# Performance work log

Measured on AMD Instinct MI355X. Metric: run time of the kernel, lower is better.

The kernel has to match this reference:

```python
import jax, jax.numpy as jnp
import numpy as np

NBINS = 100  # hard-coded in torch.histogram(first, 100)


def setup_inputs() -> dict:
    key = jax.random.key(0)
    k1, k2 = jax.random.split(key)
    z = jax.random.normal(k1, (100000, 16), dtype=jnp.float32)
    cluster_layer = jax.random.normal(k2, (16, 16), dtype=jnp.float32)
    return {"z": z, "cluster_layer": cluster_layer}


def _per_feature_hist(combined):
    """Equal-width per-feature histogram (torch.histogram(x, 100) semantics).
    combined: [N+C, F] -> edges [F, NBINS+1], counts [F, NBINS] (float)."""
    lo = combined.min(axis=0)          # [F]
    hi = combined.max(axis=0)          # [F]
    t = jnp.linspace(0.0, 1.0, NBINS + 1, dtype=combined.dtype)  # [NBINS+1]
    edges = lo[:, None] + (hi - lo)[:, None] * t[None, :]        # [F, NBINS+1]
    # bin assignment: left-closed bins, last bin right-closed (np/torch histogram)
    idx = jax.vmap(lambda e, v: jnp.searchsorted(e, v, side="right"),
                   in_axes=(0, 1))(edges, combined) - 1          # [F, N+C]
    idx = jnp.clip(idx, 0, NBINS - 1)
    counts = jax.vmap(lambda i: jnp.zeros((NBINS,), combined.dtype).at[i].add(1.0))(idx)
    return edges, counts


def _mass_dissimilarity(z, cluster_layer):
    N, F = z.shape
    C = cluster_layer.shape[0]
    combined = jax.lax.stop_gradient(jnp.concatenate([z, cluster_layer], axis=0))  # detach()
    edges, counts = _per_feature_hist(combined)          # [F,101], [F,100]

    # searchsorted(bins, .) - 1, per feature (side='left' like torch default)
    sample_bins = jax.vmap(lambda e, v: jnp.searchsorted(e, v, side="left"),
                           in_axes=(0, 1))(edges, z).T - 1              # [N, F]
    cluster_bins = jax.vmap(lambda e, v: jnp.searchsorted(e, v, side="left"),
                            in_axes=(0, 1))(edges, cluster_layer).T - 1  # [C, F]

    mx = jnp.maximum(sample_bins[:, None, :], cluster_bins[None, :, :])  # [N, C, F]
    mn = jnp.minimum(sample_bins[:, None, :], cluster_bins[None, :, :])  # [N, C, F]

    cum = jnp.cumsum(counts, axis=1)                     # [F, NBINS]
    f_idx = jnp.arange(F)                                # broadcasts over [N, C, F]
    is_zero = mn <= 0
    lo_idx = jnp.where(is_zero, 0, mn - 1)
    lo_sum = cum[f_idx, lo_idx]                          # [N, C, F]
    hi_sum = cum[f_idx, jnp.clip(mx, 0, NBINS - 1)]      # [N, C, F]
    sum_counts = jnp.where(is_zero, hi_sum, hi_sum - lo_sum)

    divisor = jnp.asarray(N + C, z.dtype)
    # len(counts)==1 in the original after reshape(1,1,F,NBINS), so no extra divide
    mass = jnp.sqrt(jnp.sum((sum_counts / divisor) ** 2, axis=2))  # [N, C]
    return mass


def reference(z, cluster_layer):
    # get_Q(z, 'mass'): q = 1/(1+mass), row-normalized
    q = 1.0 / (1.0 + _mass_dissimilarity(z, cluster_layer))
    q = q / jnp.sum(q, axis=1, keepdims=True)
    return q
```

## Files before the change

### kernel.cpp

```cpp
#include <hip/hip_runtime.h>
#include <stdint.h>

#define NBINS 100
#define FF 16
#define CC 16
#define MM_BLOCKS 256
#define HIST_BLOCKS 256


__device__ __forceinline__ unsigned enc_f(float v) {
    unsigned u = __float_as_uint(v);
    return (u & 0x80000000u) ? ~u : (u | 0x80000000u);
}
__device__ __forceinline__ float dec_f(unsigned e) {
    unsigned u = (e & 0x80000000u) ? (e ^ 0x80000000u) : ~e;
    return __uint_as_float(u);
}
__device__ __forceinline__ unsigned shfl_xor_u(unsigned x, int m) {
    return (unsigned)__shfl_xor((int)x, m, 64);
}
__device__ __forceinline__ float edgeval(float lo, float d, int k) {
    float tt = (k == NBINS) ? 1.0f : __fmul_rn((float)k, 0.01f);
    return __fadd_rn(lo, __fmul_rn(d, tt));
}

__global__ __launch_bounds__(256) void k_minmax(const float4* __restrict__ z4,
                                                const float4* __restrict__ cl4,
                                                int zn4, int total4,
                                                unsigned* __restrict__ partials,
                                                unsigned* __restrict__ counts) {
    int gtid = blockIdx.x * 256 + threadIdx.x;
    if (gtid < FF * NBINS) counts[gtid] = 0u;

    unsigned mn[4] = {~0u, ~0u, ~0u, ~0u}, mx[4] = {0u, 0u, 0u, 0u};
    int stride = MM_BLOCKS * 256;
    for (int i = gtid; i < total4; i += stride) {
        float4 v = (i < zn4) ? z4[i] : cl4[i - zn4];
        unsigned e;
        e = enc_f(v.x); mn[0] = min(mn[0], e); mx[0] = max(mx[0], e);
        e = enc_f(v.y); mn[1] = min(mn[1], e); mx[1] = max(mx[1], e);
        e = enc_f(v.z); mn[2] = min(mn[2], e); mx[2] = max(mx[2], e);
        e = enc_f(v.w); mn[3] = min(mn[3], e); mx[3] = max(mx[3], e);
    }
#pragma unroll
    for (int off = 4; off < 64; off <<= 1) {
#pragma unroll
        for (int c = 0; c < 4; ++c) {
            mn[c] = min(mn[c], shfl_xor_u(mn[c], off));
            mx[c] = max(mx[c], shfl_xor_u(mx[c], off));
        }
    }
    __shared__ unsigned smin[4][16], smax[4][16];
    int wave = threadIdx.x >> 6, lane = threadIdx.x & 63;
    if (lane < 4) {
#pragma unroll
        for (int c = 0; c < 4; ++c) {
            smin[wave][4 * lane + c] = mn[c];
            smax[wave][4 * lane + c] = mx[c];
        }
    }
    __syncthreads();
    if (threadIdx.x < 16) {
        int f = threadIdx.x;
        partials[blockIdx.x * 32 + f] =
            min(min(smin[0][f], smin[1][f]), min(smin[2][f], smin[3][f]));
        partials[blockIdx.x * 32 + 16 + f] =
            max(max(smax[0][f], smax[1][f]), max(smax[2][f], smax[3][f]));
    }
}

__global__ __launch_bounds__(256) void k_hist(const float4* __restrict__ z4,
                                              const float4* __restrict__ cl4,
                                              int zn4, int total4,
                                              const unsigned* __restrict__ partials,
                                              unsigned* __restrict__ counts,
                                              unsigned* __restrict__ sb32) {
    __shared__ unsigned ulo[16], uhi[16];
    __shared__ float slo[16], sd[16], sscl[16];
    __shared__ unsigned sc[FF * NBINS];
    int t = threadIdx.x;
    for (int i = t; i < FF * NBINS; i += 256) sc[i] = 0u;
    if (t < 16) { ulo[t] = ~0u; uhi[t] = 0u; }
    __syncthreads();
    {
        int f = t & 15, b0 = (t >> 4) * (MM_BLOCKS / 16);
        unsigned um = ~0u, ux = 0u;
#pragma unroll
        for (int b = b0; b < b0 + MM_BLOCKS / 16; ++b) {
            um = min(um, partials[b * 32 + f]);
            ux = max(ux, partials[b * 32 + 16 + f]);
        }
        atomicMin(&ulo[f], um);
        atomicMax(&uhi[f], ux);
    }
    __syncthreads();
    if (t < 16) {
        float lo = dec_f(ulo[t]), hi = dec_f(uhi[t]);
        float d = __fsub_rn(hi, lo);
        slo[t] = lo; sd[t] = d;
        sscl[t] = d > 0.0f ? 100.0f / d : 0.0f;
    }
    __syncthreads();

    int gtid = blockIdx.x * 256 + t;
    int stride = HIST_BLOCKS * 256;
    int fb = (4 * gtid) & 15;
    float lo_c[4], d_c[4], scl_c[4];
#pragma unroll
    for (int c = 0; c < 4; ++c) {
        int f = (fb + c) & 15;
        lo_c[c] = slo[f]; d_c[c] = sd[f]; scl_c[c] = sscl[f];
    }
    for (int i = gtid; i < total4; i += stride) {
        float4 v4 = (i < zn4) ? z4[i] : cl4[i - zn4];
        float vv[4] = {v4.x, v4.y, v4.z, v4.w};
        unsigned pack = 0u;
#pragma unroll
        for (int c = 0; c < 4; ++c) {
            int f = (fb + c) & 15;
            float v = vv[c], lo = lo_c[c], dd = d_c[c];
            int g = (int)((v - lo) * scl_c[c]);
            g = g < 0 ? 0 : (g > NBINS - 1 ? NBINS - 1 : g);
            while (g < NBINS - 1 && edgeval(lo, dd, g + 1) <= v) ++g;
            while (g > 0 && edgeval(lo, dd, g) > v) --g;
            atomicAdd(&sc[f * NBINS + g], 1u);
            int gl = g;
            while (gl >= 0 && edgeval(lo, dd, gl) >= v) --gl;
            pack |= ((unsigned)gl & 0xffu) << (8 * c);
        }
        sb32[i] = pack;
    }
    __syncthreads();
    for (int i = t; i < FF * NBINS; i += 256) {
        unsigned c = sc[i];
        if (c) atomicAdd(&counts[i], c);
    }
}

__global__ __launch_bounds__(256) void k_main(const signed char* __restrict__ sbins,
                                              int N, float inv_div,
                                              const unsigned* __restrict__ counts,
                                              float* __restrict__ out) {
    __shared__ unsigned scnt[FF * NBINS];
    __shared__ float scum[FF * NBINS];
    __shared__ float sqpf[CC * 32];
    int t = threadIdx.x;
    for (int i = t; i < FF * NBINS; i += 256) scnt[i] = counts[i];
    __syncthreads();
    if (t < 16) {
        float s = 0.0f;
        const unsigned* cp = &scnt[t * NBINS];
        float* fp = &scum[t * NBINS];
#pragma unroll
        for (int k = 0; k < NBINS; ++k) { s += (float)cp[k]; fp[k] = s; }
    }
    __syncthreads();
    {
        int c = t >> 4, f = t & 15;
        int g = (int)sbins[(size_t)(N + c) * FF + f];
        sqpf[c * 32 + 2 * f]     = scum[f * NBINS + (g < 0 ? 0 : g)];
        sqpf[c * 32 + 2 * f + 1] = (g >= 1) ? scum[f * NBINS + g - 1] : 0.0f;
    }
    __syncthreads();

    int n = blockIdx.x * 256 + t;
    if (n >= N) return;

    const int4* br = (const int4*)(sbins + (size_t)n * FF);
    int4 w = *br;
    int gs[FF];
    gs[0]  = (w.x << 24) >> 24; gs[1]  = (w.x << 16) >> 24;
    gs[2]  = (w.x << 8)  >> 24; gs[3]  =  w.x >> 24;
    gs[4]  = (w.y << 24) >> 24; gs[5]  = (w.y << 16) >> 24;
    gs[6]  = (w.y << 8)  >> 24; gs[7]  =  w.y >> 24;
    gs[8]  = (w.z << 24) >> 24; gs[9]  = (w.z << 16) >> 24;
    gs[10] = (w.z << 8)  >> 24; gs[11] =  w.z >> 24;
    gs[12] = (w.w << 24) >> 24; gs[13] = (w.w << 16) >> 24;
    gs[14] = (w.w << 8)  >> 24; gs[15] =  w.w >> 24;

    float Qs[FF], Ps[FF];
#pragma unroll
    for (int f = 0; f < FF; ++f) {
        int g = gs[f];
        Qs[f] = scum[f * NBINS + (g < 0 ? 0 : g)];
        Ps[f] = (g >= 1) ? scum[f * NBINS + g - 1] : 0.0f;
    }

    float q[CC];
    float rowsum = 0.0f;
#pragma unroll
    for (int c = 0; c < CC; ++c) {
        float acc = 0.0f;
        const float4* qprow = (const float4*)&sqpf[c * 32];
#pragma unroll
        for (int f2 = 0; f2 < 8; ++f2) {
            float4 qp = qprow[f2];
            float h0 = fmaxf(Qs[2 * f2], qp.x);
            float l0 = fminf(Ps[2 * f2], qp.y);
            float d0 = h0 - l0;
            acc = fmaf(d0, d0, acc);
            float h1 = fmaxf(Qs[2 * f2 + 1], qp.z);
            float l1 = fminf(Ps[2 * f2 + 1], qp.w);
            float d1 = h1 - l1;
            acc = fmaf(d1, d1, acc);
        }
        float mass = sqrtf(acc) * inv_div;
        float qq = 1.0f / (1.0f + mass);
        q[c] = qq;
        rowsum += qq;
    }

    float* op = out + (size_t)n * CC;
    float4 o;
    o.x = q[0] / rowsum;  o.y = q[1] / rowsum;  o.z = q[2] / rowsum;  o.w = q[3] / rowsum;
    ((float4*)op)[0] = o;
    o.x = q[4] / rowsum;  o.y = q[5] / rowsum;  o.z = q[6] / rowsum;  o.w = q[7] / rowsum;
    ((float4*)op)[1] = o;
    o.x = q[8] / rowsum;  o.y = q[9] / rowsum;  o.z = q[10] / rowsum; o.w = q[11] / rowsum;
    ((float4*)op)[2] = o;
    o.x = q[12] / rowsum; o.y = q[13] / rowsum; o.z = q[14] / rowsum; o.w = q[15] / rowsum;
    ((float4*)op)[3] = o;
}

extern "C" void kernel_launch(void* const* d_in, const int* in_sizes, int n_in,
                              void* d_out, int out_size, void* d_ws, size_t ws_size,
                              hipStream_t stream) {
    const float* z  = (const float*)d_in[0];
    const float* cl = (const float*)d_in[1];
    float* out = (float*)d_out;
    int N = in_sizes[0] / FF;

    char* ws = (char*)d_ws;
    unsigned*    partials = (unsigned*)(ws);
    unsigned*    counts   = (unsigned*)(ws + 32768);
    signed char* sbins    = (signed char*)(ws + 39168);

    int zn4 = N * FF / 4;
    int total4 = (N + CC) * FF / 4;
    float inv_div = 1.0f / (float)(N + CC);

    k_minmax<<<MM_BLOCKS, 256, 0, stream>>>((const float4*)z, (const float4*)cl,
                                            zn4, total4, partials, counts);
    k_hist<<<HIST_BLOCKS, 256, 0, stream>>>((const float4*)z, (const float4*)cl,
                                            zn4, total4, partials, counts,
                                            (unsigned*)sbins);
    int blocks = (N + 255) / 256;
    k_main<<<blocks, 256, 0, stream>>>(sbins, N, inv_div, counts, out);
}
```

Before: 106.4 us.

## Fuse histogram and mass kernels via grid barrier, recompute bins instead of storing

Merges the histogram and main mass kernels into one persistent kernel. A global atomic spin barrier waits for all histogram counts to be accumulated before the blocks build the cumulative sums. The per-sample searchsorted bins are no longer written to a byte buffer and read back; each sample's bins are recomputed from z in the second phase. This removes a launch and the bins round-trip through memory, but it re-reads z and repeats the bin search. It also depends on all 256 blocks being co-resident for the barrier to make progress.

```diff
diff --git a/kernel.cpp b/kernel.cpp
--- a/kernel.cpp
+++ b/kernel.cpp
@@ -4,8 +4,8 @@
 #define NBINS 100
 #define FF 16
 #define CC 16
-#define MM_BLOCKS 256
-#define HIST_BLOCKS 256
+#define GRID 256
+#define NTHREADS 256
 
 
 __device__ __forceinline__ unsigned enc_f(float v) {
@@ -28,12 +28,14 @@
                                                 const float4* __restrict__ cl4,
                                                 int zn4, int total4,
                                                 unsigned* __restrict__ partials,
-                                                unsigned* __restrict__ counts) {
-    int gtid = blockIdx.x * 256 + threadIdx.x;
+                                                unsigned* __restrict__ counts,
+                                                unsigned* __restrict__ bar) {
+    int gtid = blockIdx.x * NTHREADS + threadIdx.x;
     if (gtid < FF * NBINS) counts[gtid] = 0u;
+    if (gtid == FF * NBINS) *bar = 0u;
 
     unsigned mn[4] = {~0u, ~0u, ~0u, ~0u}, mx[4] = {0u, 0u, 0u, 0u};
-    int stride = MM_BLOCKS * 256;
+    int stride = GRID * NTHREADS;
     for (int i = gtid; i < total4; i += stride) {
         float4 v = (i < zn4) ? z4[i] : cl4[i - zn4];
         unsigned e;
@@ -69,24 +71,30 @@
     }
 }
 
-__global__ __launch_bounds__(256) void k_hist(const float4* __restrict__ z4,
-                                              const float4* __restrict__ cl4,
-                                              int zn4, int total4,
-                                              const unsigned* __restrict__ partials,
-                                              unsigned* __restrict__ counts,
-                                              unsigned* __restrict__ sb32) {
+__global__ __launch_bounds__(256) void k_rest(
+        const float4* __restrict__ z4, const float4* __restrict__ cl4,
+        int zn4, int total4, int N, float inv_div,
+        const unsigned* __restrict__ partials, unsigned* __restrict__ counts,
+        unsigned* __restrict__ bar, const float* __restrict__ cl,
+        float* __restrict__ out)
+{
     __shared__ unsigned ulo[16], uhi[16];
     __shared__ float slo[16], sd[16], sscl[16];
     __shared__ unsigned sc[FF * NBINS];
+    __shared__ float scum[FF * NBINS];
+    __shared__ float sqpf[CC * 32];
     int t = threadIdx.x;
-    for (int i = t; i < FF * NBINS; i += 256) sc[i] = 0u;
+    int gtid = blockIdx.x * NTHREADS + t;
+    int gsz = GRID * NTHREADS;
+
+    for (int i = t; i < FF * NBINS; i += NTHREADS) sc[i] = 0u;
     if (t < 16) { ulo[t] = ~0u; uhi[t] = 0u; }
     __syncthreads();
     {
-        int f = t & 15, b0 = (t >> 4) * (MM_BLOCKS / 16);
+        int f = t & 15, b0 = (t >> 4) * (GRID / 16);
         unsigned um = ~0u, ux = 0u;
 #pragma unroll
-        for (int b = b0; b < b0 + MM_BLOCKS / 16; ++b) {
+        for (int b = b0; b < b0 + GRID / 16; ++b) {
             um = min(um, partials[b * 32 + f]);
             ux = max(ux, partials[b * 32 + 16 + f]);
         }
@@ -102,8 +110,6 @@
     }
     __syncthreads();
 
-    int gtid = blockIdx.x * 256 + t;
-    int stride = HIST_BLOCKS * 256;
     int fb = (4 * gtid) & 15;
     float lo_c[4], d_c[4], scl_c[4];
 #pragma unroll
@@ -111,10 +117,9 @@
         int f = (fb + c) & 15;
         lo_c[c] = slo[f]; d_c[c] = sd[f]; scl_c[c] = sscl[f];
     }
-    for (int i = gtid; i < total4; i += stride) {
+    for (int i = gtid; i < total4; i += gsz) {
         float4 v4 = (i < zn4) ? z4[i] : cl4[i - zn4];
         float vv[4] = {v4.x, v4.y, v4.z, v4.w};
-        unsigned pack = 0u;
 #pragma unroll
         for (int c = 0; c < 4; ++c) {
             int f = (fb + c) & 15;
@@ -124,32 +129,31 @@
             while (g < NBINS - 1 && edgeval(lo, dd, g + 1) <= v) ++g;
             while (g > 0 && edgeval(lo, dd, g) > v) --g;
             atomicAdd(&sc[f * NBINS + g], 1u);
-            int gl = g;
-            while (gl >= 0 && edgeval(lo, dd, gl) >= v) --gl;
-            pack |= ((unsigned)gl & 0xffu) << (8 * c);
-        }
-        sb32[i] = pack;
-    }
-    __syncthreads();
-    for (int i = t; i < FF * NBINS; i += 256) {
+        }
+    }
+    __syncthreads();
+    for (int i = t; i < FF * NBINS; i += NTHREADS) {
         unsigned c = sc[i];
         if (c) atomicAdd(&counts[i], c);
     }
-}
-
-__global__ __launch_bounds__(256) void k_main(const signed char* __restrict__ sbins,
-                                              int N, float inv_div,
-                                              const unsigned* __restrict__ counts,
-                                              float* __restrict__ out) {
-    __shared__ unsigned scnt[FF * NBINS];
-    __shared__ float scum[FF * NBINS];
-    __shared__ float sqpf[CC * 32];
-    int t = threadIdx.x;
-    for (int i = t; i < FF * NBINS; i += 256) scnt[i] = counts[i];
+    __syncthreads();
+
+    if (t == 0) {
+        __hip_atomic_fetch_add(bar, 1u, __ATOMIC_RELEASE, __HIP_MEMORY_SCOPE_AGENT);
+        while (__hip_atomic_load(bar, __ATOMIC_ACQUIRE, __HIP_MEMORY_SCOPE_AGENT)
+               < (unsigned)GRID) {
+            __builtin_amdgcn_s_sleep(2);
+        }
+    }
+    __syncthreads();
+
+    for (int i = t; i < FF * NBINS; i += NTHREADS)
+        sc[i] = __hip_atomic_load(&counts[i], __ATOMIC_RELAXED,
+                                  __HIP_MEMORY_SCOPE_AGENT);
     __syncthreads();
     if (t < 16) {
         float s = 0.0f;
-        const unsigned* cp = &scnt[t * NBINS];
+        const unsigned* cp = &sc[t * NBINS];
         float* fp = &scum[t * NBINS];
 #pragma unroll
         for (int k = 0; k < NBINS; ++k) { s += (float)cp[k]; fp[k] = s; }
@@ -157,93 +161,95 @@
     __syncthreads();
     {
         int c = t >> 4, f = t & 15;
-        int g = (int)sbins[(size_t)(N + c) * FF + f];
+        float v = cl[c * FF + f];
+        float lo = slo[f], dd = sd[f];
+        int g = (int)((v - lo) * sscl[f]);
+        g = g < 0 ? 0 : (g > NBINS - 1 ? NBINS - 1 : g);
+        while (g < NBINS - 1 && edgeval(lo, dd, g + 1) < v) ++g;
+        while (g >= 0 && edgeval(lo, dd, g) >= v) --g;
         sqpf[c * 32 + 2 * f]     = scum[f * NBINS + (g < 0 ? 0 : g)];
         sqpf[c * 32 + 2 * f + 1] = (g >= 1) ? scum[f * NBINS + g - 1] : 0.0f;
     }
     __syncthreads();
 
-    int n = blockIdx.x * 256 + t;
-    if (n >= N) return;
-
-    const int4* br = (const int4*)(sbins + (size_t)n * FF);
-    int4 w = *br;
-    int gs[FF];
-    gs[0]  = (w.x << 24) >> 24; gs[1]  = (w.x << 16) >> 24;
-    gs[2]  = (w.x << 8)  >> 24; gs[3]  =  w.x >> 24;
-    gs[4]  = (w.y << 24) >> 24; gs[5]  = (w.y << 16) >> 24;
-    gs[6]  = (w.y << 8)  >> 24; gs[7]  =  w.y >> 24;
-    gs[8]  = (w.z << 24) >> 24; gs[9]  = (w.z << 16) >> 24;
-    gs[10] = (w.z << 8)  >> 24; gs[11] =  w.z >> 24;
-    gs[12] = (w.w << 24) >> 24; gs[13] = (w.w << 16) >> 24;
-    gs[14] = (w.w << 8)  >> 24; gs[15] =  w.w >> 24;
-
-    float Qs[FF], Ps[FF];
-#pragma unroll
-    for (int f = 0; f < FF; ++f) {
-        int g = gs[f];
-        Qs[f] = scum[f * NBINS + (g < 0 ? 0 : g)];
-        Ps[f] = (g >= 1) ? scum[f * NBINS + g - 1] : 0.0f;
-    }
-
-    float q[CC];
-    float rowsum = 0.0f;
-#pragma unroll
-    for (int c = 0; c < CC; ++c) {
-        float acc = 0.0f;
-        const float4* qprow = (const float4*)&sqpf[c * 32];
-#pragma unroll
-        for (int f2 = 0; f2 < 8; ++f2) {
-            float4 qp = qprow[f2];
-            float h0 = fmaxf(Qs[2 * f2], qp.x);
-            float l0 = fminf(Ps[2 * f2], qp.y);
-            float d0 = h0 - l0;
-            acc = fmaf(d0, d0, acc);
-            float h1 = fmaxf(Qs[2 * f2 + 1], qp.z);
-            float l1 = fminf(Ps[2 * f2 + 1], qp.w);
-            float d1 = h1 - l1;
-            acc = fmaf(d1, d1, acc);
-        }
-        float mass = sqrtf(acc) * inv_div;
-        float qq = 1.0f / (1.0f + mass);
-        q[c] = qq;
-        rowsum += qq;
-    }
-
-    float* op = out + (size_t)n * CC;
-    float4 o;
-    o.x = q[0] / rowsum;  o.y = q[1] / rowsum;  o.z = q[2] / rowsum;  o.w = q[3] / rowsum;
-    ((float4*)op)[0] = o;
-    o.x = q[4] / rowsum;  o.y = q[5] / rowsum;  o.z = q[6] / rowsum;  o.w = q[7] / rowsum;
-    ((float4*)op)[1] = o;
-    o.x = q[8] / rowsum;  o.y = q[9] / rowsum;  o.z = q[10] / rowsum; o.w = q[11] / rowsum;
-    ((float4*)op)[2] = o;
-    o.x = q[12] / rowsum; o.y = q[13] / rowsum; o.z = q[14] / rowsum; o.w = q[15] / rowsum;
-    ((float4*)op)[3] = o;
+    for (int n = gtid; n < N; n += gsz) {
+        float v[FF];
+        const float4* zr = z4 + (size_t)n * 4;
+        float4 a0 = zr[0], a1 = zr[1], a2 = zr[2], a3 = zr[3];
+        v[0] = a0.x; v[1] = a0.y; v[2]  = a0.z; v[3]  = a0.w;
+        v[4] = a1.x; v[5] = a1.y; v[6]  = a1.z; v[7]  = a1.w;
+        v[8] = a2.x; v[9] = a2.y; v[10] = a2.z; v[11] = a2.w;
+        v[12] = a3.x; v[13] = a3.y; v[14] = a3.z; v[15] = a3.w;
+
+        float Qs[FF], Ps[FF];
+#pragma unroll
+        for (int f = 0; f < FF; ++f) {
+            float lo = slo[f], dd = sd[f];
+            int g = (int)((v[f] - lo) * sscl[f]);
+            g = g < 0 ? 0 : (g > NBINS - 1 ? NBINS - 1 : g);
+            while (g < NBINS - 1 && edgeval(lo, dd, g + 1) < v[f]) ++g;
+            while (g >= 0 && edgeval(lo, dd, g) >= v[f]) --g;
+            Qs[f] = scum[f * NBINS + (g < 0 ? 0 : g)];
+            Ps[f] = (g >= 1) ? scum[f * NBINS + g - 1] : 0.0f;
+        }
+
+        float q[CC];
+        float rowsum = 0.0f;
+#pragma unroll
+        for (int c = 0; c < CC; ++c) {
+            float acc = 0.0f;
+            const float4* qprow = (const float4*)&sqpf[c * 32];
+#pragma unroll
+            for (int f2 = 0; f2 < 8; ++f2) {
+                float4 qp = qprow[f2];
+                float h0 = fmaxf(Qs[2 * f2], qp.x);
+                float l0 = fminf(Ps[2 * f2], qp.y);
+                float d0 = h0 - l0;
+                acc = fmaf(d0, d0, acc);
+                float h1 = fmaxf(Qs[2 * f2 + 1], qp.z);
+                float l1 = fminf(Ps[2 * f2 + 1], qp.w);
+                float d1 = h1 - l1;
+                acc = fmaf(d1, d1, acc);
+            }
+            float mass = sqrtf(acc) * inv_div;
+            float qq = 1.0f / (1.0f + mass);
+            q[c] = qq;
+            rowsum += qq;
+        }
+
+        float* op = out + (size_t)n * CC;
+        float4 o;
+        o.x = q[0] / rowsum;  o.y = q[1] / rowsum;  o.z = q[2] / rowsum;  o.w = q[3] / rowsum;
+        ((float4*)op)[0] = o;
+        o.x = q[4] / rowsum;  o.y = q[5] / rowsum;  o.z = q[6] / rowsum;  o.w = q[7] / rowsum;
+        ((float4*)op)[1] = o;
+        o.x = q[8] / rowsum;  o.y = q[9] / rowsum;  o.z = q[10] / rowsum; o.w = q[11] / rowsum;
+        ((float4*)op)[2] = o;
+        o.x = q[12] / rowsum; o.y = q[13] / rowsum; o.z = q[14] / rowsum; o.w = q[15] / rowsum;
+        ((float4*)op)[3] = o;
+    }
 }
 
 extern "C" void kernel_launch(void* const* d_in, const int* in_sizes, int n_in,
                               void* d_out, int out_size, void* d_ws, size_t ws_size,
                               hipStream_t stream) {
-    const float* z  = (const float*)d_in[0];
     const float* cl = (const float*)d_in[1];
     float* out = (float*)d_out;
     int N = in_sizes[0] / FF;
 
     char* ws = (char*)d_ws;
-    unsigned*    partials = (unsigned*)(ws);
-    unsigned*    counts   = (unsigned*)(ws + 32768);
-    signed char* sbins    = (signed char*)(ws + 39168);
-
+    unsigned* partials = (unsigned*)(ws);
+    unsigned* counts   = (unsigned*)(ws + 32768);
+    unsigned* bar      = (unsigned*)(ws + 39168);
+
+    const float4* z4  = (const float4*)d_in[0];
+    const float4* cl4 = (const float4*)d_in[1];
     int zn4 = N * FF / 4;
     int total4 = (N + CC) * FF / 4;
     float inv_div = 1.0f / (float)(N + CC);
 
-    k_minmax<<<MM_BLOCKS, 256, 0, stream>>>((const float4*)z, (const float4*)cl,
-                                            zn4, total4, partials, counts);
-    k_hist<<<HIST_BLOCKS, 256, 0, stream>>>((const float4*)z, (const float4*)cl,
-                                            zn4, total4, partials, counts,
-                                            (unsigned*)sbins);
-    int blocks = (N + 255) / 256;
-    k_main<<<blocks, 256, 0, stream>>>(sbins, N, inv_div, counts, out);
-}
+    k_minmax<<<GRID, NTHREADS, 0, stream>>>(z4, cl4, zn4, total4,
+                                            partials, counts, bar);
+    k_rest<<<GRID, NTHREADS, 0, stream>>>(z4, cl4, zn4, total4, N, inv_div,
+                                          partials, counts, bar, cl, out);
+}
```

After: 124.7 us. 1.17x slower.

## Recompute sample bins in main kernel and split cluster work across threads

Applied to the files above, without the earlier changes.

The histogram kernel no longer writes packed per-sample left-side bin indices. The main kernel now reloads z and recomputes each bin directly from min/lo and scale parameters that the first histogram block stores. The main kernel also changes its work split: 16 threads per sample, one per cluster, with Q/P values staged in shared memory and the row sum done by shuffles. Block sizes of the min/max and histogram kernels grow to 1024 threads. This removes the byte-index write and read at the cost of a second pass over z and extra blocks, each of which recomputes the cumulative histogram.

```diff
diff --git a/kernel.cpp b/kernel.cpp
--- a/kernel.cpp
+++ b/kernel.cpp
@@ -5,7 +5,11 @@
 #define FF 16
 #define CC 16
 #define MM_BLOCKS 256
-#define HIST_BLOCKS 256
+#define MM_THREADS 1024
+#define H_BLOCKS 256
+#define H_THREADS 1024
+#define SPB 64
+#define M_THREADS 256
 
 
 __device__ __forceinline__ unsigned enc_f(float v) {
@@ -24,16 +28,17 @@
     return __fadd_rn(lo, __fmul_rn(d, tt));
 }
 
-__global__ __launch_bounds__(256) void k_minmax(const float4* __restrict__ z4,
-                                                const float4* __restrict__ cl4,
-                                                int zn4, int total4,
-                                                unsigned* __restrict__ partials,
-                                                unsigned* __restrict__ counts) {
-    int gtid = blockIdx.x * 256 + threadIdx.x;
+__global__ __launch_bounds__(1024) void k_minmax(const float4* __restrict__ z4,
+                                                 const float4* __restrict__ cl4,
+                                                 int zn4, int total4,
+                                                 unsigned* __restrict__ partials,
+                                                 unsigned* __restrict__ counts) {
+    int t = threadIdx.x;
+    int gtid = blockIdx.x * MM_THREADS + t;
     if (gtid < FF * NBINS) counts[gtid] = 0u;
 
     unsigned mn[4] = {~0u, ~0u, ~0u, ~0u}, mx[4] = {0u, 0u, 0u, 0u};
-    int stride = MM_BLOCKS * 256;
+    int stride = MM_BLOCKS * MM_THREADS;
     for (int i = gtid; i < total4; i += stride) {
         float4 v = (i < zn4) ? z4[i] : cl4[i - zn4];
         unsigned e;
@@ -50,8 +55,8 @@
             mx[c] = max(mx[c], shfl_xor_u(mx[c], off));
         }
     }
-    __shared__ unsigned smin[4][16], smax[4][16];
-    int wave = threadIdx.x >> 6, lane = threadIdx.x & 63;
+    __shared__ unsigned smin[16][16], smax[16][16];
+    int wave = t >> 6, lane = t & 63;
     if (lane < 4) {
 #pragma unroll
         for (int c = 0; c < 4; ++c) {
@@ -60,33 +65,36 @@
         }
     }
     __syncthreads();
-    if (threadIdx.x < 16) {
-        int f = threadIdx.x;
-        partials[blockIdx.x * 32 + f] =
-            min(min(smin[0][f], smin[1][f]), min(smin[2][f], smin[3][f]));
-        partials[blockIdx.x * 32 + 16 + f] =
-            max(max(smax[0][f], smax[1][f]), max(smax[2][f], smax[3][f]));
-    }
-}
-
-__global__ __launch_bounds__(256) void k_hist(const float4* __restrict__ z4,
-                                              const float4* __restrict__ cl4,
-                                              int zn4, int total4,
-                                              const unsigned* __restrict__ partials,
-                                              unsigned* __restrict__ counts,
-                                              unsigned* __restrict__ sb32) {
+    if (t < 16) {
+        unsigned um = ~0u, ux = 0u;
+#pragma unroll
+        for (int w = 0; w < 16; ++w) {
+            um = min(um, smin[w][t]);
+            ux = max(ux, smax[w][t]);
+        }
+        partials[blockIdx.x * 32 + t] = um;
+        partials[blockIdx.x * 32 + 16 + t] = ux;
+    }
+}
+
+__global__ __launch_bounds__(1024) void k_hist(const float4* __restrict__ z4,
+                                               const float4* __restrict__ cl4,
+                                               int zn4, int total4,
+                                               const unsigned* __restrict__ partials,
+                                               unsigned* __restrict__ counts,
+                                               float* __restrict__ params) {
     __shared__ unsigned ulo[16], uhi[16];
     __shared__ float slo[16], sd[16], sscl[16];
     __shared__ unsigned sc[FF * NBINS];
     int t = threadIdx.x;
-    for (int i = t; i < FF * NBINS; i += 256) sc[i] = 0u;
+    for (int i = t; i < FF * NBINS; i += H_THREADS) sc[i] = 0u;
     if (t < 16) { ulo[t] = ~0u; uhi[t] = 0u; }
     __syncthreads();
     {
-        int f = t & 15, b0 = (t >> 4) * (MM_BLOCKS / 16);
+        int f = t & 15, b0 = (t >> 4) * (MM_BLOCKS / 64);
         unsigned um = ~0u, ux = 0u;
 #pragma unroll
-        for (int b = b0; b < b0 + MM_BLOCKS / 16; ++b) {
+        for (int b = b0; b < b0 + MM_BLOCKS / 64; ++b) {
             um = min(um, partials[b * 32 + f]);
             ux = max(ux, partials[b * 32 + 16 + f]);
         }
@@ -99,11 +107,14 @@
         float d = __fsub_rn(hi, lo);
         slo[t] = lo; sd[t] = d;
         sscl[t] = d > 0.0f ? 100.0f / d : 0.0f;
-    }
-    __syncthreads();
-
-    int gtid = blockIdx.x * 256 + t;
-    int stride = HIST_BLOCKS * 256;
+        if (blockIdx.x == 0) {
+            params[t] = lo; params[16 + t] = d; params[32 + t] = sscl[t];
+        }
+    }
+    __syncthreads();
+
+    int gtid = blockIdx.x * H_THREADS + t;
+    int stride = H_BLOCKS * H_THREADS;
     int fb = (4 * gtid) & 15;
     float lo_c[4], d_c[4], scl_c[4];
 #pragma unroll
@@ -114,7 +125,6 @@
     for (int i = gtid; i < total4; i += stride) {
         float4 v4 = (i < zn4) ? z4[i] : cl4[i - zn4];
         float vv[4] = {v4.x, v4.y, v4.z, v4.w};
-        unsigned pack = 0u;
 #pragma unroll
         for (int c = 0; c < 4; ++c) {
             int f = (fb + c) & 15;
@@ -124,102 +134,94 @@
             while (g < NBINS - 1 && edgeval(lo, dd, g + 1) <= v) ++g;
             while (g > 0 && edgeval(lo, dd, g) > v) --g;
             atomicAdd(&sc[f * NBINS + g], 1u);
-            int gl = g;
-            while (gl >= 0 && edgeval(lo, dd, gl) >= v) --gl;
-            pack |= ((unsigned)gl & 0xffu) << (8 * c);
-        }
-        sb32[i] = pack;
-    }
-    __syncthreads();
-    for (int i = t; i < FF * NBINS; i += 256) {
+        }
+    }
+    __syncthreads();
+    for (int i = t; i < FF * NBINS; i += H_THREADS) {
         unsigned c = sc[i];
         if (c) atomicAdd(&counts[i], c);
     }
 }
 
-__global__ __launch_bounds__(256) void k_main(const signed char* __restrict__ sbins,
-                                              int N, float inv_div,
+__global__ __launch_bounds__(256) void k_main(const float* __restrict__ z, int N,
+                                              float inv_div,
                                               const unsigned* __restrict__ counts,
+                                              const float* __restrict__ params,
+                                              const float* __restrict__ cl,
                                               float* __restrict__ out) {
-    __shared__ unsigned scnt[FF * NBINS];
+    __shared__ float sparam[48];
+    __shared__ unsigned sc[FF * NBINS];
     __shared__ float scum[FF * NBINS];
-    __shared__ float sqpf[CC * 32];
+    __shared__ float2 sqs[SPB * 17];
+    __shared__ float2 sqp[FF * CC];
     int t = threadIdx.x;
-    for (int i = t; i < FF * NBINS; i += 256) scnt[i] = counts[i];
+    for (int i = t; i < FF * NBINS; i += M_THREADS) sc[i] = counts[i];
+    if (t < 48) sparam[t] = params[t];
     __syncthreads();
     if (t < 16) {
         float s = 0.0f;
-        const unsigned* cp = &scnt[t * NBINS];
+        const unsigned* cp = &sc[t * NBINS];
         float* fp = &scum[t * NBINS];
 #pragma unroll
         for (int k = 0; k < NBINS; ++k) { s += (float)cp[k]; fp[k] = s; }
     }
     __syncthreads();
     {
-        int c = t >> 4, f = t & 15;
-        int g = (int)sbins[(size_t)(N + c) * FF + f];
-        sqpf[c * 32 + 2 * f]     = scum[f * NBINS + (g < 0 ? 0 : g)];
-        sqpf[c * 32 + 2 * f + 1] = (g >= 1) ? scum[f * NBINS + g - 1] : 0.0f;
-    }
-    __syncthreads();
-
-    int n = blockIdx.x * 256 + t;
-    if (n >= N) return;
-
-    const int4* br = (const int4*)(sbins + (size_t)n * FF);
-    int4 w = *br;
-    int gs[FF];
-    gs[0]  = (w.x << 24) >> 24; gs[1]  = (w.x << 16) >> 24;
-    gs[2]  = (w.x << 8)  >> 24; gs[3]  =  w.x >> 24;
-    gs[4]  = (w.y << 24) >> 24; gs[5]  = (w.y << 16) >> 24;
-    gs[6]  = (w.y << 8)  >> 24; gs[7]  =  w.y >> 24;
-    gs[8]  = (w.z << 24) >> 24; gs[9]  = (w.z << 16) >> 24;
-    gs[10] = (w.z << 8)  >> 24; gs[11] =  w.z >> 24;
-    gs[12] = (w.w << 24) >> 24; gs[13] = (w.w << 16) >> 24;
-    gs[14] = (w.w << 8)  >> 24; gs[15] =  w.w >> 24;
-
-    float Qs[FF], Ps[FF];
-#pragma unroll
-    for (int f = 0; f < FF; ++f) {
-        int g = gs[f];
-        Qs[f] = scum[f * NBINS + (g < 0 ? 0 : g)];
-        Ps[f] = (g >= 1) ? scum[f * NBINS + g - 1] : 0.0f;
-    }
-
-    float q[CC];
-    float rowsum = 0.0f;
-#pragma unroll
-    for (int c = 0; c < CC; ++c) {
-        float acc = 0.0f;
-        const float4* qprow = (const float4*)&sqpf[c * 32];
-#pragma unroll
-        for (int f2 = 0; f2 < 8; ++f2) {
-            float4 qp = qprow[f2];
-            float h0 = fmaxf(Qs[2 * f2], qp.x);
-            float l0 = fminf(Ps[2 * f2], qp.y);
-            float d0 = h0 - l0;
-            acc = fmaf(d0, d0, acc);
-            float h1 = fmaxf(Qs[2 * f2 + 1], qp.z);
-            float l1 = fminf(Ps[2 * f2 + 1], qp.w);
-            float d1 = h1 - l1;
-            acc = fmaf(d1, d1, acc);
-        }
-        float mass = sqrtf(acc) * inv_div;
-        float qq = 1.0f / (1.0f + mass);
-        q[c] = qq;
-        rowsum += qq;
-    }
-
-    float* op = out + (size_t)n * CC;
-    float4 o;
-    o.x = q[0] / rowsum;  o.y = q[1] / rowsum;  o.z = q[2] / rowsum;  o.w = q[3] / rowsum;
-    ((float4*)op)[0] = o;
-    o.x = q[4] / rowsum;  o.y = q[5] / rowsum;  o.z = q[6] / rowsum;  o.w = q[7] / rowsum;
-    ((float4*)op)[1] = o;
-    o.x = q[8] / rowsum;  o.y = q[9] / rowsum;  o.z = q[10] / rowsum; o.w = q[11] / rowsum;
-    ((float4*)op)[2] = o;
-    o.x = q[12] / rowsum; o.y = q[13] / rowsum; o.z = q[14] / rowsum; o.w = q[15] / rowsum;
-    ((float4*)op)[3] = o;
+        int c = t & 15, f = t >> 4;
+        float v = cl[c * FF + f];
+        float lo = sparam[f], dd = sparam[16 + f];
+        int g = (int)((v - lo) * sparam[32 + f]);
+        g = g < 0 ? 0 : (g > NBINS - 1 ? NBINS - 1 : g);
+        while (g < NBINS - 1 && edgeval(lo, dd, g + 1) < v) ++g;
+        while (g >= 0 && edgeval(lo, dd, g) >= v) --g;
+        float Qc = scum[f * NBINS + (g < 0 ? 0 : g)];
+        float Pc = (g >= 1) ? scum[f * NBINS + g - 1] : 0.0f;
+        sqp[f * CC + c] = make_float2(Qc, Pc);
+    }
+    int n0 = blockIdx.x * SPB;
+#pragma unroll
+    for (int ns = 0; ns < SPB / 16; ++ns) {
+        int nl = ns * 16 + (t >> 4), f = t & 15;
+        int n = n0 + nl;
+        if (n < N) {
+            float v = z[(size_t)n * FF + f];
+            float lo = sparam[f], dd = sparam[16 + f];
+            int g = (int)((v - lo) * sparam[32 + f]);
+            g = g < 0 ? 0 : (g > NBINS - 1 ? NBINS - 1 : g);
+            while (g < NBINS - 1 && edgeval(lo, dd, g + 1) < v) ++g;
+            while (g >= 0 && edgeval(lo, dd, g) >= v) --g;
+            float Qs = scum[f * NBINS + (g < 0 ? 0 : g)];
+            float Ps = (g >= 1) ? scum[f * NBINS + g - 1] : 0.0f;
+            sqs[nl * 17 + f] = make_float2(Qs, Ps);
+        }
+    }
+    __syncthreads();
+
+#pragma unroll
+    for (int ns = 0; ns < SPB / 16; ++ns) {
+        int nl = ns * 16 + (t >> 4), c = t & 15;
+        int n = n0 + nl;
+        if (n < N) {
+            float acc = 0.0f;
+#pragma unroll
+            for (int f = 0; f < FF; ++f) {
+                float2 s = sqs[nl * 17 + f];
+                float2 p = sqp[f * CC + c];
+                float h = fmaxf(s.x, p.x);
+                float l = fminf(s.y, p.y);
+                float d = h - l;
+                acc = fmaf(d, d, acc);
+            }
+            float mass = sqrtf(acc) * inv_div;
+            float qq = 1.0f / (1.0f + mass);
+            float rs = qq;
+            rs += __shfl_xor(rs, 1, 64);
+            rs += __shfl_xor(rs, 2, 64);
+            rs += __shfl_xor(rs, 4, 64);
+            rs += __shfl_xor(rs, 8, 64);
+            out[(size_t)n * CC + c] = qq / rs;
+        }
+    }
 }
 
 extern "C" void kernel_launch(void* const* d_in, const int* in_sizes, int n_in,
@@ -231,19 +233,21 @@
     int N = in_sizes[0] / FF;
 
     char* ws = (char*)d_ws;
-    unsigned*    partials = (unsigned*)(ws);
-    unsigned*    counts   = (unsigned*)(ws + 32768);
-    signed char* sbins    = (signed char*)(ws + 39168);
-
+    unsigned* partials = (unsigned*)(ws);
+    unsigned* counts   = (unsigned*)(ws + 32768);
+    float*    params   = (float*)(ws + 39168);
+
+    const float4* z4  = (const float4*)d_in[0];
+    const float4* cl4 = (const float4*)d_in[1];
     int zn4 = N * FF / 4;
     int total4 = (N + CC) * FF / 4;
     float inv_div = 1.0f / (float)(N + CC);
 
-    k_minmax<<<MM_BLOCKS, 256, 0, stream>>>((const float4*)z, (const float4*)cl,
-                                            zn4, total4, partials, counts);
-    k_hist<<<HIST_BLOCKS, 256, 0, stream>>>((const float4*)z, (const float4*)cl,
-                                            zn4, total4, partials, counts,
-                                            (unsigned*)sbins);
-    int blocks = (N + 255) / 256;
-    k_main<<<blocks, 256, 0, stream>>>(sbins, N, inv_div, counts, out);
-}
+    k_minmax<<<MM_BLOCKS, MM_THREADS, 0, stream>>>(z4, cl4, zn4, total4,
+                                                   partials, counts);
+    k_hist<<<H_BLOCKS, H_THREADS, 0, stream>>>(z4, cl4, zn4, total4,
+                                               partials, counts, params);
+    int mblocks = (N + SPB - 1) / SPB;
+    k_main<<<mblocks, M_THREADS, 0, stream>>>(z, N, inv_div, counts, params,
+                                              cl, out);
+}
```

Result: faster. 98.65 us (-7.3%).
